# Performance work log

Measured on AMD Instinct MI355X. Metric: run time of the kernel, lower is better.

The kernel has to match this reference:

```python
import jax, jax.numpy as jnp
import numpy as np

N = 50000      # nodes
E = 800000     # edges
HID = 128      # hidden_dim (== input_dim)
HEADS = 4
D = HID // HEADS  # 32 head dim
L = 3          # n_layers
G = 64         # graphs in batch
LAT = 64       # latent_dim


def _segment_softmax(logits, seg, num):
    # logits: [E, HEADS], seg: [E] -> softmax over edges sharing the same dst node
    m = jax.ops.segment_max(logits, seg, num_segments=num)          # [N, HEADS]
    e = jnp.exp(logits - m[seg])
    s = jax.ops.segment_sum(e, seg, num_segments=num)               # [N, HEADS]
    return e / (s[seg] + 1e-16)


def setup_inputs() -> dict:
    key = jax.random.key(0)
    ks = jax.random.split(key, 16)
    sc = 0.05
    inp = {
        "x": jax.random.normal(ks[0], (N, HID), dtype=jnp.float32),
        "edge_index": jax.random.randint(ks[1], (2, E), 0, N, dtype=jnp.int32),
        "batch": jnp.sort(jax.random.randint(ks[2], (N,), 0, G, dtype=jnp.int32)),
        # input projection
        "Win": jax.random.normal(ks[3], (HID, HID), dtype=jnp.float32) * sc,
        "bin_": jnp.zeros((HID,), dtype=jnp.float32),
        # per-layer TransformerConv params (stacked over layers)
        "Wq": jax.random.normal(ks[4], (L, HID, HID), dtype=jnp.float32) * sc,
        "bq": jnp.zeros((L, HID), dtype=jnp.float32),
        "Wk": jax.random.normal(ks[5], (L, HID, HID), dtype=jnp.float32) * sc,
        "bk": jnp.zeros((L, HID), dtype=jnp.float32),
        "Wv": jax.random.normal(ks[6], (L, HID, HID), dtype=jnp.float32) * sc,
        "bv": jnp.zeros((L, HID), dtype=jnp.float32),
        "Wskip": jax.random.normal(ks[7], (L, HID, HID), dtype=jnp.float32) * sc,
        "bskip": jnp.zeros((L, HID), dtype=jnp.float32),
        # final fc
        "Wfc": jax.random.normal(ks[8], (LAT, HID), dtype=jnp.float32) * sc,
        "bfc": jnp.zeros((LAT,), dtype=jnp.float32),
    }
    return inp


def reference(x, edge_index, batch, Win, bin_, Wq, bq, Wk, bk, Wv, bv, Wskip, bskip, Wfc, bfc):
    src, dst = edge_index[0], edge_index[1]
    h = x @ Win.T + bin_                                   # [N, HID]
    scale = 1.0 / np.sqrt(D).astype(np.float32)
    for l in range(L):
        q = (h @ Wq[l].T + bq[l]).reshape(N, HEADS, D)
        k = (h @ Wk[l].T + bk[l]).reshape(N, HEADS, D)
        v = (h @ Wv[l].T + bv[l]).reshape(N, HEADS, D)
        # edge-level gather: query at dst, key/value at src
        alpha = jnp.einsum('ehd,ehd->eh', q[dst], k[src]) * scale   # [E, HEADS]
        a = _segment_softmax(alpha, dst, N)                          # [E, HEADS]
        msg = a[..., None] * v[src]                                  # [E, HEADS, D]
        out = jax.ops.segment_sum(msg, dst, num_segments=N).reshape(N, HID)
        h = jax.nn.relu(out + h @ Wskip[l].T + bskip[l])            # root (skip) connection, then ReLU
    pooled = jax.ops.segment_sum(h, batch, num_segments=G)          # global_add_pool -> [G, HID]
    return pooled @ Wfc.T + bfc                                      # [G, LAT]
```

## Files before the change

kernel.cpp:

```cpp
#include <hip/hip_runtime.h>
#include <math.h>

#define NN 50000
#define NE 800000
#define HID 128
#define NL 3
#define NG 64
#define LAT 64

typedef __attribute__((ext_vector_type(8))) short short8v;
typedef __attribute__((ext_vector_type(4))) short short4v;
typedef __attribute__((ext_vector_type(4))) float f32x4;
typedef __attribute__((ext_vector_type(2))) float f32x2;

__device__ __forceinline__ float bf2f(unsigned short b) {
    unsigned u = ((unsigned)b) << 16;
    return __builtin_bit_cast(float, u);
}
__device__ __forceinline__ unsigned short f2bf(float f) {
    unsigned u = __builtin_bit_cast(unsigned, f);
    u += 0x7FFFu + ((u >> 16) & 1u);
    return (unsigned short)(u >> 16);
}

__device__ __forceinline__ float dot8_fp8(int d0, int d1, const float* qf) {
    f32x2 a01 = __builtin_amdgcn_cvt_pk_f32_fp8(d0, false);
    f32x2 a23 = __builtin_amdgcn_cvt_pk_f32_fp8(d0, true);
    f32x2 a45 = __builtin_amdgcn_cvt_pk_f32_fp8(d1, false);
    f32x2 a67 = __builtin_amdgcn_cvt_pk_f32_fp8(d1, true);
    return a01[0]*qf[0] + a01[1]*qf[1] + a23[0]*qf[2] + a23[1]*qf[3]
         + a45[0]*qf[4] + a45[1]*qf[5] + a67[0]*qf[6] + a67[1]*qf[7];
}
__device__ __forceinline__ void acc8_fp8(int d0, int d1, float wgt, float* acc) {
    f32x2 v01 = __builtin_amdgcn_cvt_pk_f32_fp8(d0, false);
    f32x2 v23 = __builtin_amdgcn_cvt_pk_f32_fp8(d0, true);
    f32x2 v45 = __builtin_amdgcn_cvt_pk_f32_fp8(d1, false);
    f32x2 v67 = __builtin_amdgcn_cvt_pk_f32_fp8(d1, true);
    acc[0] += wgt * v01[0]; acc[1] += wgt * v01[1];
    acc[2] += wgt * v23[0]; acc[3] += wgt * v23[1];
    acc[4] += wgt * v45[0]; acc[5] += wgt * v45[1];
    acc[6] += wgt * v67[0]; acc[7] += wgt * v67[1];
}

struct PtrTab { const float* p[13]; };

__global__ __launch_bounds__(256) void pack_all_kernel(
    PtrTab wt, PtrTab bt, short* __restrict__ Wcat, short* __restrict__ Wt,
    float* __restrict__ bcat, int* __restrict__ deg, float* __restrict__ pooled)
{
    int gid = blockIdx.x * 256 + threadIdx.x;
    if (gid < 16384) {
        Wcat[gid] = (short)f2bf(wt.p[0][gid]);
    }
    if (gid < 12 * 16384) {
        int i  = gid & 7;
        int c  = (gid >> 3) & 511;
        int kb = (gid >> 12) & 15;
        int l  = gid >> 16;
        int slot = 1 + 4 * l + (c >> 7);
        int elem = (c & 127) * 128 + kb * 8 + i;
        Wt[gid] = (short)f2bf(wt.p[slot][elem]);
    }
    if (gid < 13 * 128) {
        int slot = gid >> 7, e = gid & 127;
        bcat[gid] = bt.p[slot][e];
    }
    if (gid < NN) deg[gid] = 0;
    if (gid < NG * HID) pooled[gid] = 0.f;
}

__global__ __launch_bounds__(512) void gemm_layer(
    const short* __restrict__ A, const short* __restrict__ Wt_l,
    const float* __restrict__ bias, short* __restrict__ qs,
    signed char* __restrict__ kv8, int nrows)
{
    constexpr int CSTR = 516;
    __shared__ short Clds[16 * CSTR];

    const int tid  = threadIdx.x;
    const int lane = tid & 63;
    const int wid  = tid >> 6;
    const int n0   = wid * 64;
    const int lg   = lane >> 4;
    const int l15  = lane & 15;
    const int rb   = blockIdx.x * 64;
    const int r0   = rb + l15;

    f32x4 acc[4][4];
#pragma unroll
    for (int i = 0; i < 4; ++i)
#pragma unroll
        for (int j = 0; j < 4; ++j) acc[i][j] = {0.f, 0.f, 0.f, 0.f};

    const short8v zero8 = {0, 0, 0, 0, 0, 0, 0, 0};

#pragma unroll
    for (int s = 0; s < 4; ++s) {
        short8v a[4], b[4];
#pragma unroll
        for (int mf = 0; mf < 4; ++mf) {
            int row = r0 + mf * 16;
            a[mf] = (row < nrows)
                ? *reinterpret_cast<const short8v*>(&A[(size_t)row * HID + s * 32 + lg * 8])
                : zero8;
        }
        const int kb = s * 4 + lg;
#pragma unroll
        for (int nf = 0; nf < 4; ++nf) {
            int col = n0 + nf * 16 + l15;
            b[nf] = *reinterpret_cast<const short8v*>(&Wt_l[((size_t)kb * 512 + col) * 8]);
        }
#pragma unroll
        for (int mf = 0; mf < 4; ++mf)
#pragma unroll
            for (int nf = 0; nf < 4; ++nf)
                acc[mf][nf] = __builtin_amdgcn_mfma_f32_16x16x32_bf16(
                    a[mf], b[nf], acc[mf][nf], 0, 0, 0);
    }

#pragma unroll
    for (int mf = 0; mf < 4; ++mf) {
        __syncthreads();
#pragma unroll
        for (int nf = 0; nf < 4; ++nf) {
            int col = n0 + nf * 16 + l15;
            float bv = bias[col];
#pragma unroll
            for (int qq = 0; qq < 4; ++qq) {
                int rl = lg * 4 + qq;
                Clds[rl * CSTR + col] = (short)f2bf(acc[mf][nf][qq] + bv);
            }
        }
        __syncthreads();
#pragma unroll
        for (int i = 0; i < 2; ++i) {
            int c = tid + 512 * i;
            int rl = c >> 6;
            int ck = c & 63;
            int grow = rb + mf * 16 + rl;
            if (grow < nrows) {
                if (ck < 16) {
                    *reinterpret_cast<short8v*>(&qs[(size_t)grow * 256 + ck * 8]) =
                        *reinterpret_cast<const short8v*>(&Clds[rl * CSTR + ck * 8]);
                } else if (ck < 48) {
                    short8v cv = *reinterpret_cast<const short8v*>(&Clds[rl * CSTR + ck * 8]);
                    float f0 = bf2f((unsigned short)cv[0]), f1 = bf2f((unsigned short)cv[1]);
                    float f2 = bf2f((unsigned short)cv[2]), f3 = bf2f((unsigned short)cv[3]);
                    float f4 = bf2f((unsigned short)cv[4]), f5 = bf2f((unsigned short)cv[5]);
                    float f6 = bf2f((unsigned short)cv[6]), f7 = bf2f((unsigned short)cv[7]);
                    int w0 = __builtin_amdgcn_cvt_pk_fp8_f32(f0, f1, 0, false);
                    w0     = __builtin_amdgcn_cvt_pk_fp8_f32(f2, f3, w0, true);
                    int w1 = __builtin_amdgcn_cvt_pk_fp8_f32(f4, f5, 0, false);
                    w1     = __builtin_amdgcn_cvt_pk_fp8_f32(f6, f7, w1, true);
                    int off = (ck < 32) ? (ck - 16) * 16 : ((ck - 32) * 16 + 8);
                    *reinterpret_cast<int2*>(kv8 + (size_t)grow * 256 + off) =
                        make_int2(w0, w1);
                } else {
                    *reinterpret_cast<short8v*>(&qs[(size_t)grow * 256 + 128 + (ck - 48) * 8]) =
                        *reinterpret_cast<const short8v*>(&Clds[rl * CSTR + ck * 8]);
                }
            }
        }
    }
}

__global__ __launch_bounds__(256, 2) void gemm_in(
    const float* __restrict__ Af, const short* __restrict__ Wcat,
    const float* __restrict__ bias, short* __restrict__ out, int nrows)
{
    constexpr int CSTR = 132;
    __shared__ short smem[16 * 128 * 8];
    short* Wlds = smem;
    short* Clds = smem;

    const int tid  = threadIdx.x;
    const int lane = tid & 63;
    const int wid  = tid >> 6;
    const int blockbase = blockIdx.x * 256;
    const int rbase = blockbase + wid * 64;
    const int r0 = rbase + (lane & 15);
    const int lg = lane >> 4;

    for (int c = tid; c < 128 * 16; c += 256) {
        int j = c & 127;
        int kb = c >> 7;
        *reinterpret_cast<short8v*>(&Wlds[(kb * 128 + j) * 8]) =
            *reinterpret_cast<const short8v*>(&Wcat[j * HID + kb * 8]);
    }
    __syncthreads();

    f32x4 acc[4][8];
#pragma unroll
    for (int i = 0; i < 4; ++i)
#pragma unroll
        for (int j = 0; j < 8; ++j) acc[i][j] = {0.f, 0.f, 0.f, 0.f};

    const short8v zero8 = {0, 0, 0, 0, 0, 0, 0, 0};
    for (int s = 0; s < 4; ++s) {
        short8v a[4], b[8];
#pragma unroll
        for (int mf = 0; mf < 4; ++mf) {
            int row = r0 + mf * 16;
            if (row < nrows) {
                const float* ap = Af + (size_t)row * HID + s * 32 + lg * 8;
                float4 f0 = *reinterpret_cast<const float4*>(ap);
                float4 f1 = *reinterpret_cast<const float4*>(ap + 4);
                short8v t;
                t[0] = (short)f2bf(f0.x); t[1] = (short)f2bf(f0.y);
                t[2] = (short)f2bf(f0.z); t[3] = (short)f2bf(f0.w);
                t[4] = (short)f2bf(f1.x); t[5] = (short)f2bf(f1.y);
                t[6] = (short)f2bf(f1.z); t[7] = (short)f2bf(f1.w);
                a[mf] = t;
            } else a[mf] = zero8;
        }
        const int kb = s * 4 + lg;
#pragma unroll
        for (int nf = 0; nf < 8; ++nf) {
            int slot = kb * 128 + nf * 16 + (lane & 15);
            b[nf] = *reinterpret_cast<const short8v*>(&Wlds[slot * 8]);
        }
#pragma unroll
        for (int mf = 0; mf < 4; ++mf)
#pragma unroll
            for (int nf = 0; nf < 8; ++nf)
                acc[mf][nf] = __builtin_amdgcn_mfma_f32_16x16x32_bf16(
                    a[mf], b[nf], acc[mf][nf], 0, 0, 0);
    }

#pragma unroll
    for (int mf = 0; mf < 4; ++mf) {
        __syncthreads();
#pragma unroll
        for (int nf = 0; nf < 8; ++nf) {
            int col = nf * 16 + (lane & 15);
            float bv = bias[col];
#pragma unroll
            for (int qq = 0; qq < 4; ++qq) {
                int rl = wid * 4 + lg;
                (void)rl;
                Clds[(wid * 16 + lg * 4 + qq) * CSTR + col] =
                    (short)f2bf(acc[mf][nf][qq] + bv);
            }
        }
        __syncthreads();
#pragma unroll
        for (int i = 0; i < 4; ++i) {
            int c = tid + 256 * i;
            int rl = c >> 4;
            int ck = c & 15;
            int grow = blockbase + (rl >> 4) * 64 + mf * 16 + (rl & 15);
            if (grow < nrows)
                *reinterpret_cast<short8v*>(&out[(size_t)grow * HID + ck * 8]) =
                    *reinterpret_cast<const short8v*>(&Clds[rl * CSTR + ck * 8]);
        }
    }
}

__global__ __launch_bounds__(256) void count_deg_kernel(
    const int* __restrict__ dst, int* __restrict__ deg,
    unsigned short* __restrict__ rank16, int ne)
{
    int e = blockIdx.x * 256 + threadIdx.x;
    if (e < ne) {
        int r = atomicAdd(&deg[dst[e]], 1);
        rank16[e] = (unsigned short)r;
    }
}

__global__ __launch_bounds__(1024) void scan1_kernel(
    const int* __restrict__ deg, int* __restrict__ offsets,
    int* __restrict__ bsum, int n)
{
    __shared__ int wsum[16];
    const int tid = threadIdx.x, wid = tid >> 6, lane = tid & 63;
    int i = blockIdx.x * 1024 + tid;
    int val = (i < n) ? deg[i] : 0;
    int x = val;
#pragma unroll
    for (int off = 1; off < 64; off <<= 1) {
        int y = __shfl_up(x, off);
        if (lane >= off) x += y;
    }
    if (lane == 63) wsum[wid] = x;
    __syncthreads();
    if (tid < 16) {
        int w = wsum[tid];
#pragma unroll
        for (int off = 1; off < 16; off <<= 1) {
            int y = __shfl_up(w, off);
            if (tid >= off) w += y;
        }
        wsum[tid] = w;
    }
    __syncthreads();
    int incl = x + (wid ? wsum[wid - 1] : 0);
    if (i < n) offsets[i + 1] = incl;
    if (tid == 1023) bsum[blockIdx.x] = incl;
}

__global__ __launch_bounds__(256) void scan3_kernel(
    int* __restrict__ offsets, const int* __restrict__ bsum, int n, int nb)
{
    __shared__ int sx[64];
    const int tid = threadIdx.x;
    if (tid < 64) {
        int vv = (tid < nb) ? bsum[tid] : 0;
        int x = vv;
#pragma unroll
        for (int off = 1; off < 64; off <<= 1) {
            int y = __shfl_up(x, off);
            if (tid >= off) x += y;
        }
        sx[tid] = x - vv;
    }
    __syncthreads();
    int i = blockIdx.x * 256 + tid;
    if (i >= n) return;
    offsets[i + 1] += sx[i >> 10];
    if (i == 0) offsets[0] = 0;
}

__global__ __launch_bounds__(256) void scatter_kernel(
    const int* __restrict__ src, const int* __restrict__ dst,
    const int* __restrict__ offsets, const unsigned short* __restrict__ rank16,
    unsigned short* __restrict__ csr16, int ne)
{
    int e = blockIdx.x * 256 + threadIdx.x;
    if (e < ne) {
        int pos = offsets[dst[e]] + rank16[e];
        csr16[pos] = (unsigned short)src[e];
    }
}

__global__ __launch_bounds__(256) void attn_kernel(
    const short* __restrict__ qs, const signed char* __restrict__ kv8,
    const int* __restrict__ offsets, const unsigned short* __restrict__ csr16,
    short* __restrict__ hout, int nnodes)
{
    int node = (blockIdx.x * 256 + threadIdx.x) >> 6;
    if (node >= nnodes) return;
    const int lane = threadIdx.x & 63;
    const int grp = lane >> 4;
    const int g   = lane & 15;
    const float scale = 0.17677669529663687f;

    const size_t nb = (size_t)node * 256;
    short8v q8 = *reinterpret_cast<const short8v*>(&qs[nb + g * 8]);
    float qf[8];
#pragma unroll
    for (int i = 0; i < 8; ++i) qf[i] = bf2f((unsigned short)q8[i]);

    int e0 = offsets[node], e1 = offsets[node + 1];
    float s = 0.f;
    float acc[8] = {0.f, 0.f, 0.f, 0.f, 0.f, 0.f, 0.f, 0.f};

    const signed char* kvb = kv8 + g * 16;

    int e = e0 + grp;
    int i0 = (e < e1)     ? (int)csr16[e]     : 0;
    int i1 = (e + 4 < e1) ? (int)csr16[e + 4] : 0;

    for (; e + 4 < e1; e += 8) {
        int j0 = (e + 8  < e1) ? (int)csr16[e + 8]  : 0;
        int j1 = (e + 12 < e1) ? (int)csr16[e + 12] : 0;
        int4 kv0 = *reinterpret_cast<const int4*>(kvb + ((size_t)i0 << 8));
        int4 kv1 = *reinterpret_cast<const int4*>(kvb + ((size_t)i1 << 8));
        float p0 = dot8_fp8(kv0.x, kv0.y, qf);
        float p1 = dot8_fp8(kv1.x, kv1.y, qf);
        p0 += __shfl_xor(p0, 1);  p1 += __shfl_xor(p1, 1);
        p0 += __shfl_xor(p0, 2);  p1 += __shfl_xor(p1, 2);
        float w0 = __expf(fminf(p0 * scale, 60.f));
        float w1 = __expf(fminf(p1 * scale, 60.f));
        s += w0 + w1;
        acc8_fp8(kv0.z, kv0.w, w0, acc);
        acc8_fp8(kv1.z, kv1.w, w1, acc);
        i0 = j0; i1 = j1;
    }
    if (e < e1) {
        int4 kv0 = *reinterpret_cast<const int4*>(kvb + ((size_t)i0 << 8));
        float p0 = dot8_fp8(kv0.x, kv0.y, qf);
        p0 += __shfl_xor(p0, 1);
        p0 += __shfl_xor(p0, 2);
        float w0 = __expf(fminf(p0 * scale, 60.f));
        s += w0;
        acc8_fp8(kv0.z, kv0.w, w0, acc);
    }

#pragma unroll
    for (int off = 16; off <= 32; off <<= 1) {
        s += __shfl_xor(s, off);
#pragma unroll
        for (int i = 0; i < 8; ++i) acc[i] += __shfl_xor(acc[i], off);
    }
    float inv = 1.f / (s + 1e-16f);
    short8v sk8 = *reinterpret_cast<const short8v*>(&qs[nb + 128 + g * 8]);
    short8v o;
#pragma unroll
    for (int i = 0; i < 8; ++i) {
        float ov = fmaxf(acc[i] * inv + bf2f((unsigned short)sk8[i]), 0.f);
        o[i] = (short)f2bf(ov);
    }
    *reinterpret_cast<short8v*>(&hout[(size_t)node * HID + g * 8]) = o;
}

__global__ __launch_bounds__(256) void pool_kernel(
    const short* __restrict__ h, const int* __restrict__ batch,
    float* __restrict__ pooled, int nnodes)
{
    const int ROWS = 256;
    int n0 = blockIdx.x * ROWS;
    if (n0 >= nnodes) return;
    int n1 = min(n0 + ROWS, nnodes);
    int rg = threadIdx.x >> 5;
    int c4 = threadIdx.x & 31;
    float s0 = 0.f, s1 = 0.f, s2 = 0.f, s3 = 0.f;
    int g = -1;
    for (int n = n0 + rg; n < n1; n += 8) {
        int bg = batch[n];
        if (bg != g) {
            if (g >= 0) {
                atomicAdd(&pooled[g * HID + c4 * 4 + 0], s0);
                atomicAdd(&pooled[g * HID + c4 * 4 + 1], s1);
                atomicAdd(&pooled[g * HID + c4 * 4 + 2], s2);
                atomicAdd(&pooled[g * HID + c4 * 4 + 3], s3);
            }
            s0 = s1 = s2 = s3 = 0.f;
            g = bg;
        }
        short4v hv = *reinterpret_cast<const short4v*>(&h[(size_t)n * HID + c4 * 4]);
        s0 += bf2f((unsigned short)hv[0]);
        s1 += bf2f((unsigned short)hv[1]);
        s2 += bf2f((unsigned short)hv[2]);
        s3 += bf2f((unsigned short)hv[3]);
    }
    if (g >= 0) {
        atomicAdd(&pooled[g * HID + c4 * 4 + 0], s0);
        atomicAdd(&pooled[g * HID + c4 * 4 + 1], s1);
        atomicAdd(&pooled[g * HID + c4 * 4 + 2], s2);
        atomicAdd(&pooled[g * HID + c4 * 4 + 3], s3);
    }
}

__global__ __launch_bounds__(256) void fc_kernel(
    const float* __restrict__ pooled, const float* __restrict__ Wfc,
    const float* __restrict__ bfc, float* __restrict__ out)
{
    int t = blockIdx.x * 256 + threadIdx.x;
    if (t >= NG * LAT) return;
    int g = t >> 6, o = t & 63;
    float sum = bfc[o];
    for (int j = 0; j < HID; ++j)
        sum += pooled[g * HID + j] * Wfc[o * HID + j];
    out[t] = sum;
}

extern "C" void kernel_launch(void* const* d_in, const int* in_sizes, int n_in,
                              void* d_out, int out_size, void* d_ws, size_t ws_size,
                              hipStream_t stream)
{
    const float* x     = (const float*)d_in[0];
    const int*   ei    = (const int*)d_in[1];
    const int*   batch = (const int*)d_in[2];
    const float* Win   = (const float*)d_in[3];
    const float* bin_  = (const float*)d_in[4];
    const float* Wq    = (const float*)d_in[5];
    const float* bq    = (const float*)d_in[6];
    const float* Wk    = (const float*)d_in[7];
    const float* bk    = (const float*)d_in[8];
    const float* Wv    = (const float*)d_in[9];
    const float* bv    = (const float*)d_in[10];
    const float* Wskip = (const float*)d_in[11];
    const float* bskip = (const float*)d_in[12];
    const float* Wfc   = (const float*)d_in[13];
    const float* bfc   = (const float*)d_in[14];
    float* out = (float*)d_out;

    char* ws = (char*)d_ws;
    auto alloc = [&](size_t bytes) {
        void* p = (void*)ws;
        ws += (bytes + 255) & ~(size_t)255;
        return p;
    };
    short* hb     = (short*)alloc((size_t)NN * HID * 2);
    short* qs     = (short*)alloc((size_t)NN * 256 * 2);
    signed char* kv8 = (signed char*)alloc((size_t)NN * 256);
    short* Wcat   = (short*)alloc((size_t)16384 * 2);
    short* Wt     = (short*)alloc((size_t)12 * 16384 * 2);
    float* bcat   = (float*)alloc((size_t)13 * 128 * 4);
    float* pooled = (float*)alloc((size_t)NG * HID * 4);
    int* deg      = (int*)alloc((size_t)NN * 4);
    int* offsets  = (int*)alloc((size_t)(NN + 1) * 4);
    int* bsum     = (int*)alloc((size_t)64 * 4);
    unsigned short* rank16 = (unsigned short*)alloc((size_t)NE * 2);
    unsigned short* csr16  = (unsigned short*)alloc((size_t)NE * 2);

    const int* esrc = ei;
    const int* edst = ei + NE;

    PtrTab wt, bt;
    wt.p[0] = Win; bt.p[0] = bin_;
    for (int l = 0; l < NL; ++l) {
        wt.p[1 + 4 * l] = Wq    + (size_t)l * HID * HID;
        wt.p[2 + 4 * l] = Wk    + (size_t)l * HID * HID;
        wt.p[3 + 4 * l] = Wv    + (size_t)l * HID * HID;
        wt.p[4 + 4 * l] = Wskip + (size_t)l * HID * HID;
        bt.p[1 + 4 * l] = bq    + (size_t)l * HID;
        bt.p[2 + 4 * l] = bk    + (size_t)l * HID;
        bt.p[3 + 4 * l] = bv    + (size_t)l * HID;
        bt.p[4 + 4 * l] = bskip + (size_t)l * HID;
    }

    pack_all_kernel<<<(12 * 16384 + 255) / 256, 256, 0, stream>>>(
        wt, bt, Wcat, Wt, bcat, deg, pooled);

    const int egrid = (NE + 255) / 256;
    const int nsb = (NN + 1023) / 1024;
    count_deg_kernel<<<egrid, 256, 0, stream>>>(edst, deg, rank16, NE);
    scan1_kernel<<<nsb, 1024, 0, stream>>>(deg, offsets, bsum, NN);
    scan3_kernel<<<(NN + 255) / 256, 256, 0, stream>>>(offsets, bsum, NN, nsb);
    scatter_kernel<<<egrid, 256, 0, stream>>>(esrc, edst, offsets, rank16, csr16, NE);

    gemm_in<<<(NN + 255) / 256, 256, 0, stream>>>(x, Wcat, bcat, hb, NN);

    const int gl = (NN + 63) / 64;
    for (int l = 0; l < NL; ++l) {
        gemm_layer<<<gl, 512, 0, stream>>>(
            hb, Wt + (size_t)l * 16 * 512 * 8, bcat + (1 + 4 * l) * 128, qs, kv8, NN);
        attn_kernel<<<(NN + 3) / 4, 256, 0, stream>>>(qs, kv8, offsets, csr16, hb, NN);
    }

    pool_kernel<<<(NN + 255) / 256, 256, 0, stream>>>(hb, batch, pooled, NN);
    fc_kernel<<<16, 256, 0, stream>>>(pooled, Wfc, bfc, out);
}
```

Measured before the change: 295.0 us.

## Retile input GEMM to 64-row blocks reading pre-packed weights from global

The input projection GEMM is retiled. Each block now handles 64 rows with 128 threads, and each wave computes a 64-column slice. Weights are pre-packed in MFMA fragment order and read straight from global memory (L2) instead of being staged through LDS, which removes the LDS weight-load phase and the extra sync, shrinks LDS use and launches more blocks. The pool kernel switches to 16-byte loads over 128-row blocks, and the FC kernel uses float4 loads. The tradeoff is more redundant global weight reads and more pool atomics.

```diff
diff --git a/kernel.cpp b/kernel.cpp
--- a/kernel.cpp
+++ b/kernel.cpp
@@ -45,12 +45,15 @@
 struct PtrTab { const float* p[13]; };
 
 __global__ __launch_bounds__(256) void pack_all_kernel(
-    PtrTab wt, PtrTab bt, short* __restrict__ Wcat, short* __restrict__ Wt,
+    PtrTab wt, PtrTab bt, short* __restrict__ Wt0, short* __restrict__ Wt,
     float* __restrict__ bcat, int* __restrict__ deg, float* __restrict__ pooled)
 {
     int gid = blockIdx.x * 256 + threadIdx.x;
     if (gid < 16384) {
-        Wcat[gid] = (short)f2bf(wt.p[0][gid]);
+        int i  = gid & 7;
+        int j  = (gid >> 3) & 127;
+        int kb = gid >> 10;
+        Wt0[gid] = (short)f2bf(wt.p[0][j * 128 + kb * 8 + i]);
     }
     if (gid < 12 * 16384) {
         int i  = gid & 7;
@@ -164,40 +167,33 @@
     }
 }
 
-__global__ __launch_bounds__(256, 2) void gemm_in(
-    const float* __restrict__ Af, const short* __restrict__ Wcat,
+__global__ __launch_bounds__(128) void gemm_in(
+    const float* __restrict__ Af, const short* __restrict__ Wt0,
     const float* __restrict__ bias, short* __restrict__ out, int nrows)
 {
     constexpr int CSTR = 132;
-    __shared__ short smem[16 * 128 * 8];
-    short* Wlds = smem;
-    short* Clds = smem;
+    __shared__ short Clds[16 * CSTR];
 
     const int tid  = threadIdx.x;
     const int lane = tid & 63;
     const int wid  = tid >> 6;
-    const int blockbase = blockIdx.x * 256;
-    const int rbase = blockbase + wid * 64;
-    const int r0 = rbase + (lane & 15);
-    const int lg = lane >> 4;
-
-    for (int c = tid; c < 128 * 16; c += 256) {
-        int j = c & 127;
-        int kb = c >> 7;
-        *reinterpret_cast<short8v*>(&Wlds[(kb * 128 + j) * 8]) =
-            *reinterpret_cast<const short8v*>(&Wcat[j * HID + kb * 8]);
-    }
-    __syncthreads();
-
-    f32x4 acc[4][8];
+    const int n0   = wid * 64;
+    const int lg   = lane >> 4;
+    const int l15  = lane & 15;
+    const int rb   = blockIdx.x * 64;
+    const int r0   = rb + l15;
+
+    f32x4 acc[4][4];
 #pragma unroll
     for (int i = 0; i < 4; ++i)
 #pragma unroll
-        for (int j = 0; j < 8; ++j) acc[i][j] = {0.f, 0.f, 0.f, 0.f};
+        for (int j = 0; j < 4; ++j) acc[i][j] = {0.f, 0.f, 0.f, 0.f};
 
     const short8v zero8 = {0, 0, 0, 0, 0, 0, 0, 0};
+
+#pragma unroll
     for (int s = 0; s < 4; ++s) {
-        short8v a[4], b[8];
+        short8v a[4], b[4];
 #pragma unroll
         for (int mf = 0; mf < 4; ++mf) {
             int row = r0 + mf * 16;
@@ -215,14 +211,14 @@
         }
         const int kb = s * 4 + lg;
 #pragma unroll
-        for (int nf = 0; nf < 8; ++nf) {
-            int slot = kb * 128 + nf * 16 + (lane & 15);
-            b[nf] = *reinterpret_cast<const short8v*>(&Wlds[slot * 8]);
+        for (int nf = 0; nf < 4; ++nf) {
+            int col = n0 + nf * 16 + l15;
+            b[nf] = *reinterpret_cast<const short8v*>(&Wt0[((size_t)kb * 128 + col) * 8]);
         }
 #pragma unroll
         for (int mf = 0; mf < 4; ++mf)
 #pragma unroll
-            for (int nf = 0; nf < 8; ++nf)
+            for (int nf = 0; nf < 4; ++nf)
                 acc[mf][nf] = __builtin_amdgcn_mfma_f32_16x16x32_bf16(
                     a[mf], b[nf], acc[mf][nf], 0, 0, 0);
     }
@@ -231,24 +227,22 @@
     for (int mf = 0; mf < 4; ++mf) {
         __syncthreads();
 #pragma unroll
-        for (int nf = 0; nf < 8; ++nf) {
-            int col = nf * 16 + (lane & 15);
+        for (int nf = 0; nf < 4; ++nf) {
+            int col = n0 + nf * 16 + l15;
             float bv = bias[col];
 #pragma unroll
             for (int qq = 0; qq < 4; ++qq) {
-                int rl = wid * 4 + lg;
-                (void)rl;
-                Clds[(wid * 16 + lg * 4 + qq) * CSTR + col] =
-                    (short)f2bf(acc[mf][nf][qq] + bv);
+                int rl = lg * 4 + qq;
+                Clds[rl * CSTR + col] = (short)f2bf(acc[mf][nf][qq] + bv);
             }
         }
         __syncthreads();
 #pragma unroll
-        for (int i = 0; i < 4; ++i) {
-            int c = tid + 256 * i;
+        for (int i = 0; i < 2; ++i) {
+            int c = tid + 128 * i;
             int rl = c >> 4;
             int ck = c & 15;
-            int grow = blockbase + (rl >> 4) * 64 + mf * 16 + (rl & 15);
+            int grow = rb + mf * 16 + rl;
             if (grow < nrows)
                 *reinterpret_cast<short8v*>(&out[(size_t)grow * HID + ck * 8]) =
                     *reinterpret_cast<const short8v*>(&Clds[rl * CSTR + ck * 8]);
@@ -407,37 +401,34 @@
     const short* __restrict__ h, const int* __restrict__ batch,
     float* __restrict__ pooled, int nnodes)
 {
-    const int ROWS = 256;
+    const int ROWS = 128;
     int n0 = blockIdx.x * ROWS;
     if (n0 >= nnodes) return;
     int n1 = min(n0 + ROWS, nnodes);
-    int rg = threadIdx.x >> 5;
-    int c4 = threadIdx.x & 31;
-    float s0 = 0.f, s1 = 0.f, s2 = 0.f, s3 = 0.f;
+    int rg = threadIdx.x >> 4;
+    int c8 = threadIdx.x & 15;
+    float s[8] = {0.f, 0.f, 0.f, 0.f, 0.f, 0.f, 0.f, 0.f};
     int g = -1;
-    for (int n = n0 + rg; n < n1; n += 8) {
+    for (int n = n0 + rg; n < n1; n += 16) {
         int bg = batch[n];
         if (bg != g) {
             if (g >= 0) {
-                atomicAdd(&pooled[g * HID + c4 * 4 + 0], s0);
-                atomicAdd(&pooled[g * HID + c4 * 4 + 1], s1);
-                atomicAdd(&pooled[g * HID + c4 * 4 + 2], s2);
-                atomicAdd(&pooled[g * HID + c4 * 4 + 3], s3);
+#pragma unroll
+                for (int i = 0; i < 8; ++i) {
+                    atomicAdd(&pooled[g * HID + c8 * 8 + i], s[i]);
+                    s[i] = 0.f;
+                }
             }
-            s0 = s1 = s2 = s3 = 0.f;
             g = bg;
         }
-        short4v hv = *reinterpret_cast<const short4v*>(&h[(size_t)n * HID + c4 * 4]);
-        s0 += bf2f((unsigned short)hv[0]);
-        s1 += bf2f((unsigned short)hv[1]);
-        s2 += bf2f((unsigned short)hv[2]);
-        s3 += bf2f((unsigned short)hv[3]);
+        short8v hv = *reinterpret_cast<const short8v*>(&h[(size_t)n * HID + c8 * 8]);
+#pragma unroll
+        for (int i = 0; i < 8; ++i) s[i] += bf2f((unsigned short)hv[i]);
     }
     if (g >= 0) {
-        atomicAdd(&pooled[g * HID + c4 * 4 + 0], s0);
-        atomicAdd(&pooled[g * HID + c4 * 4 + 1], s1);
-        atomicAdd(&pooled[g * HID + c4 * 4 + 2], s2);
-        atomicAdd(&pooled[g * HID + c4 * 4 + 3], s3);
+#pragma unroll
+        for (int i = 0; i < 8; ++i)
+            atomicAdd(&pooled[g * HID + c8 * 8 + i], s[i]);
     }
 }
 
@@ -449,8 +440,11 @@
     if (t >= NG * LAT) return;
     int g = t >> 6, o = t & 63;
     float sum = bfc[o];
-    for (int j = 0; j < HID; ++j)
-        sum += pooled[g * HID + j] * Wfc[o * HID + j];
+    for (int j = 0; j < HID; j += 4) {
+        float4 p = *reinterpret_cast<const float4*>(&pooled[g * HID + j]);
+        float4 w = *reinterpret_cast<const float4*>(&Wfc[o * HID + j]);
+        sum += p.x * w.x + p.y * w.y + p.z * w.z + p.w * w.w;
+    }
     out[t] = sum;
 }
 
@@ -484,7 +478,7 @@
     short* hb     = (short*)alloc((size_t)NN * HID * 2);
     short* qs     = (short*)alloc((size_t)NN * 256 * 2);
     signed char* kv8 = (signed char*)alloc((size_t)NN * 256);
-    short* Wcat   = (short*)alloc((size_t)16384 * 2);
+    short* Wt0    = (short*)alloc((size_t)16384 * 2);
     short* Wt     = (short*)alloc((size_t)12 * 16384 * 2);
     float* bcat   = (float*)alloc((size_t)13 * 128 * 4);
     float* pooled = (float*)alloc((size_t)NG * HID * 4);
@@ -511,7 +505,7 @@
     }
 
     pack_all_kernel<<<(12 * 16384 + 255) / 256, 256, 0, stream>>>(
-        wt, bt, Wcat, Wt, bcat, deg, pooled);
+        wt, bt, Wt0, Wt, bcat, deg, pooled);
 
     const int egrid = (NE + 255) / 256;
     const int nsb = (NN + 1023) / 1024;
@@ -520,15 +514,15 @@
     scan3_kernel<<<(NN + 255) / 256, 256, 0, stream>>>(offsets, bsum, NN, nsb);
     scatter_kernel<<<egrid, 256, 0, stream>>>(esrc, edst, offsets, rank16, csr16, NE);
 
-    gemm_in<<<(NN + 255) / 256, 256, 0, stream>>>(x, Wcat, bcat, hb, NN);
-
     const int gl = (NN + 63) / 64;
+    gemm_in<<<gl, 128, 0, stream>>>(x, Wt0, bcat, hb, NN);
+
     for (int l = 0; l < NL; ++l) {
         gemm_layer<<<gl, 512, 0, stream>>>(
             hb, Wt + (size_t)l * 16 * 512 * 8, bcat + (1 + 4 * l) * 128, qs, kv8, NN);
         attn_kernel<<<(NN + 3) / 4, 256, 0, stream>>>(qs, kv8, offsets, csr16, hb, NN);
     }
 
-    pool_kernel<<<(NN + 255) / 256, 256, 0, stream>>>(hb, batch, pooled, NN);
+    pool_kernel<<<(NN + 127) / 128, 256, 0, stream>>>(hb, batch, pooled, NN);
     fc_kernel<<<16, 256, 0, stream>>>(pooled, Wfc, bfc, out);
 }
```

Result: slower. 334.9 us (+13.5%).
